# Kernel optimization log

Measured on AMD Instinct MI355X. Metric: run time of the kernel, lower is better.

The kernel has to match this reference:

```python
import jax, jax.numpy as jnp
import numpy as np

L = 30  # SSA window size (module default)


def _ssa_groups1(xm):
    """pyts-style SSA with groups=1: full-SVD reconstruction of the
    trajectory (Hankel) matrix followed by anti-diagonal averaging.
    xm: [B, N] -> [B, N]
    """
    B, N = xm.shape
    K = N - L + 1
    # Hankel trajectory matrix: X[b, i, j] = xm[b, i + j], shape [B, L, K]
    idx = jnp.arange(L)[:, None] + jnp.arange(K)[None, :]
    X = xm[:, idx]
    # SVD and rank-L reconstruction (groups=1 sums ALL elementary matrices)
    U, s, Vt = jnp.linalg.svd(X, full_matrices=False)  # U:[B,L,L] s:[B,L] Vt:[B,L,K]
    Xr = jnp.einsum('blr,br,brk->blk', U, s, Vt)       # [B, L, K]
    # Anti-diagonal (Hankel) averaging: average Xr[i, j] over i + j = t
    seg = idx.reshape(-1)                               # [L*K] values in [0, N)
    sums = jax.vmap(lambda m: jax.ops.segment_sum(m.reshape(-1), seg, num_segments=N))(Xr)
    counts = jax.ops.segment_sum(jnp.ones(L * K, dtype=xm.dtype), seg, num_segments=N)
    return sums / counts                                # [B, N]


def setup_inputs() -> dict:
    key = jax.random.key(0)
    x = jax.random.normal(key, (256, 64, 2048), dtype=jnp.float32)
    return {"x": x}


def reference(x):
    # x: [B, C, N]
    xm = jnp.max(x, axis=1)                 # channel-max, [B, N]
    x_ss = _ssa_groups1(xm)                 # SSA round-trip, [B, N]
    # Original code detaches the SSA branch (CPU/numpy round trip)
    x_ss = jax.lax.stop_gradient(x_ss)
    gate = jax.nn.softmax(x_ss, axis=-1)[:, None, :]  # [B, 1, N]
    return gate * x                         # [B, C, N]
```

## Files before the change

kernel.cpp:

```cpp
#include <hip/hip_runtime.h>
#include <math.h>


#define B_DIM 256
#define C_DIM 64
#define N_DIM 2048
#define COLS4 (N_DIM / 4)
#define ROW4  (C_DIM * COLS4)

__global__ __launch_bounds__(1024)
void gate_kernel(const float* __restrict__ x, float* __restrict__ out) {
    const int b    = blockIdx.x;
    const int t    = threadIdx.x;
    const int col  = t & (COLS4 - 1);
    const int grp  = t >> 9;
    const int lane = t & 63;
    const int wid  = t >> 6;

    const float4* __restrict__ xb = (const float4*)x + (size_t)b * ROW4;
    float4* ob = (float4*)out + (size_t)b * ROW4;

    __shared__ float4 pm[2][COLS4];
    __shared__ float  sred[16];

    const int c0 = grp * 32;
    float4 m = make_float4(-INFINITY, -INFINITY, -INFINITY, -INFINITY);
    #pragma unroll 8
    for (int c = 0; c < 32; ++c) {
        float4 v = xb[(size_t)(c0 + c) * COLS4 + col];
        m.x = fmaxf(m.x, v.x); m.y = fmaxf(m.y, v.y);
        m.z = fmaxf(m.z, v.z); m.w = fmaxf(m.w, v.w);
    }
    pm[grp][col] = m;
    __syncthreads();

    float4 e;
    if (t < COLS4) {
        float4 a  = pm[0][t];
        float4 c2 = pm[1][t];
        e.x = fmaxf(a.x, c2.x); e.y = fmaxf(a.y, c2.y);
        e.z = fmaxf(a.z, c2.z); e.w = fmaxf(a.w, c2.w);
        float tm = fmaxf(fmaxf(e.x, e.y), fmaxf(e.z, e.w));
        #pragma unroll
        for (int off = 32; off > 0; off >>= 1)
            tm = fmaxf(tm, __shfl_down(tm, off, 64));
        if (lane == 0) sred[wid] = tm;
    }
    __syncthreads();
    float M = sred[0];
    #pragma unroll
    for (int i = 1; i < 8; ++i) M = fmaxf(M, sred[i]);

    if (t < COLS4) {
        e.x = __expf(e.x - M); e.y = __expf(e.y - M);
        e.z = __expf(e.z - M); e.w = __expf(e.w - M);
        float ts = (e.x + e.y) + (e.z + e.w);
        #pragma unroll
        for (int off = 32; off > 0; off >>= 1)
            ts += __shfl_down(ts, off, 64);
        if (lane == 0) sred[8 + wid] = ts;
    }
    __syncthreads();

    if (t < COLS4) {
        float S = 0.0f;
        #pragma unroll
        for (int i = 8; i < 16; ++i) S += sred[i];
        const float inv = 1.0f / S;
        float4 gg;
        gg.x = e.x * inv; gg.y = e.y * inv; gg.z = e.z * inv; gg.w = e.w * inv;
        ob[(size_t)( 0) * COLS4 + t] = gg;
        ob[(size_t)(16) * COLS4 + t] = gg;
        ob[(size_t)(32) * COLS4 + t] = gg;
        ob[(size_t)(48) * COLS4 + t] = gg;
    }
}

__global__ __launch_bounds__(512)
void mul_kernel(const float* __restrict__ x, float* __restrict__ out) {
    const int bid = blockIdx.x;
    const int b   = bid >> 2;
    const int g   = bid & 3;
    const int col = threadIdx.x;

    const size_t rbase = (size_t)b * ROW4;
    const float4* __restrict__ x4 = (const float4*)x + rbase;
    float4* o4 = (float4*)out + rbase;

    const int cbase = g * 16;
    const float4 gv = o4[(size_t)cbase * COLS4 + col];
    __syncthreads();

    #pragma unroll 4
    for (int c = 0; c < 16; ++c) {
        const size_t idx = (size_t)(cbase + c) * COLS4 + col;
        float4 v = x4[idx];
        float4 o;
        o.x = v.x * gv.x; o.y = v.y * gv.y;
        o.z = v.z * gv.z; o.w = v.w * gv.w;
        o4[idx] = o;
    }
}

extern "C" void kernel_launch(void* const* d_in, const int* in_sizes, int n_in,
                              void* d_out, int out_size, void* d_ws, size_t ws_size,
                              hipStream_t stream) {
    const float* x = (const float*)d_in[0];
    float* out = (float*)d_out;
    gate_kernel<<<B_DIM, 1024, 0, stream>>>(x, out);
    mul_kernel<<<B_DIM * 4, 512, 0, stream>>>(x, out);
}
```

Measured before the change: 250.2 us.

## Fuse gate and multiply kernels, caching x in registers and LDS

```diff
diff --git a/kernel.cpp b/kernel.cpp
--- a/kernel.cpp
+++ b/kernel.cpp
@@ -8,97 +8,116 @@
 #define COLS4 (N_DIM / 4)
 #define ROW4  (C_DIM * COLS4)
 
-__global__ __launch_bounds__(1024)
-void gate_kernel(const float* __restrict__ x, float* __restrict__ out) {
+#define REGS_CH 16
+#define LDS_CH  3
+#define RR_CH   13
+
+__global__ __launch_bounds__(1024, 4)
+void ssa_gate_fused(const float* __restrict__ x, float* __restrict__ out) {
     const int b    = blockIdx.x;
     const int t    = threadIdx.x;
     const int col  = t & (COLS4 - 1);
     const int grp  = t >> 9;
     const int lane = t & 63;
     const int wid  = t >> 6;
+    const int c0   = grp * 32;
 
     const float4* __restrict__ xb = (const float4*)x + (size_t)b * ROW4;
-    float4* ob = (float4*)out + (size_t)b * ROW4;
+    float4* __restrict__ ob = (float4*)out + (size_t)b * ROW4;
 
-    __shared__ float4 pm[2][COLS4];
-    __shared__ float  sred[16];
+    __shared__ float4 ldsx[2][LDS_CH][COLS4];
+    __shared__ float4 xmbuf[COLS4];
+    __shared__ float  sredM[16];
+    __shared__ float  sredS[16];
 
-    const int c0 = grp * 32;
+    float4 r[REGS_CH];
     float4 m = make_float4(-INFINITY, -INFINITY, -INFINITY, -INFINITY);
-    #pragma unroll 8
-    for (int c = 0; c < 32; ++c) {
-        float4 v = xb[(size_t)(c0 + c) * COLS4 + col];
+    #pragma unroll
+    for (int c = 0; c < REGS_CH; ++c) {
+        r[c] = xb[(size_t)(c0 + c) * COLS4 + col];
+        m.x = fmaxf(m.x, r[c].x); m.y = fmaxf(m.y, r[c].y);
+        m.z = fmaxf(m.z, r[c].z); m.w = fmaxf(m.w, r[c].w);
+    }
+    #pragma unroll
+    for (int k = 0; k < LDS_CH; ++k) {
+        float4 v = xb[(size_t)(c0 + REGS_CH + k) * COLS4 + col];
+        ldsx[grp][k][col] = v;
         m.x = fmaxf(m.x, v.x); m.y = fmaxf(m.y, v.y);
         m.z = fmaxf(m.z, v.z); m.w = fmaxf(m.w, v.w);
     }
-    pm[grp][col] = m;
+    #pragma unroll
+    for (int k = 0; k < RR_CH; ++k) {
+        float4 v = xb[(size_t)(c0 + REGS_CH + LDS_CH + k) * COLS4 + col];
+        m.x = fmaxf(m.x, v.x); m.y = fmaxf(m.y, v.y);
+        m.z = fmaxf(m.z, v.z); m.w = fmaxf(m.w, v.w);
+    }
+
+    if (grp == 1) xmbuf[col] = m;
     __syncthreads();
 
     float4 e;
-    if (t < COLS4) {
-        float4 a  = pm[0][t];
-        float4 c2 = pm[1][t];
-        e.x = fmaxf(a.x, c2.x); e.y = fmaxf(a.y, c2.y);
-        e.z = fmaxf(a.z, c2.z); e.w = fmaxf(a.w, c2.w);
-        float tm = fmaxf(fmaxf(e.x, e.y), fmaxf(e.z, e.w));
-        #pragma unroll
-        for (int off = 32; off > 0; off >>= 1)
-            tm = fmaxf(tm, __shfl_down(tm, off, 64));
-        if (lane == 0) sred[wid] = tm;
+    float tm = -INFINITY;
+    if (grp == 0) {
+        float4 o = xmbuf[col];
+        e.x = fmaxf(m.x, o.x); e.y = fmaxf(m.y, o.y);
+        e.z = fmaxf(m.z, o.z); e.w = fmaxf(m.w, o.w);
+        tm = fmaxf(fmaxf(e.x, e.y), fmaxf(e.z, e.w));
+    }
+    #pragma unroll
+    for (int off = 32; off > 0; off >>= 1)
+        tm = fmaxf(tm, __shfl_down(tm, off, 64));
+    if (lane == 0) sredM[wid] = tm;
+    __syncthreads();
+    float M = sredM[0];
+    #pragma unroll
+    for (int i = 1; i < 16; ++i) M = fmaxf(M, sredM[i]);
+
+    float ts = 0.0f;
+    if (grp == 0) {
+        e.x = __expf(e.x - M); e.y = __expf(e.y - M);
+        e.z = __expf(e.z - M); e.w = __expf(e.w - M);
+        ts = (e.x + e.y) + (e.z + e.w);
+    }
+    #pragma unroll
+    for (int off = 32; off > 0; off >>= 1)
+        ts += __shfl_down(ts, off, 64);
+    if (lane == 0) sredS[wid] = ts;
+    __syncthreads();
+    float S = 0.0f;
+    #pragma unroll
+    for (int i = 0; i < 16; ++i) S += sredS[i];
+
+    if (grp == 0) {
+        const float inv = 1.0f / S;
+        float4 g;
+        g.x = e.x * inv; g.y = e.y * inv; g.z = e.z * inv; g.w = e.w * inv;
+        xmbuf[col] = g;
     }
     __syncthreads();
-    float M = sred[0];
+    const float4 g = xmbuf[col];
+
     #pragma unroll
-    for (int i = 1; i < 8; ++i) M = fmaxf(M, sred[i]);
-
-    if (t < COLS4) {
-        e.x = __expf(e.x - M); e.y = __expf(e.y - M);
-        e.z = __expf(e.z - M); e.w = __expf(e.w - M);
-        float ts = (e.x + e.y) + (e.z + e.w);
-        #pragma unroll
-        for (int off = 32; off > 0; off >>= 1)
-            ts += __shfl_down(ts, off, 64);
-        if (lane == 0) sred[8 + wid] = ts;
+    for (int c = 0; c < REGS_CH; ++c) {
+        float4 w;
+        w.x = r[c].x * g.x; w.y = r[c].y * g.y;
+        w.z = r[c].z * g.z; w.w = r[c].w * g.w;
+        ob[(size_t)(c0 + c) * COLS4 + col] = w;
     }
-    __syncthreads();
-
-    if (t < COLS4) {
-        float S = 0.0f;
-        #pragma unroll
-        for (int i = 8; i < 16; ++i) S += sred[i];
-        const float inv = 1.0f / S;
-        float4 gg;
-        gg.x = e.x * inv; gg.y = e.y * inv; gg.z = e.z * inv; gg.w = e.w * inv;
-        ob[(size_t)( 0) * COLS4 + t] = gg;
-        ob[(size_t)(16) * COLS4 + t] = gg;
-        ob[(size_t)(32) * COLS4 + t] = gg;
-        ob[(size_t)(48) * COLS4 + t] = gg;
+    #pragma unroll
+    for (int k = 0; k < LDS_CH; ++k) {
+        float4 v = ldsx[grp][k][col];
+        float4 w;
+        w.x = v.x * g.x; w.y = v.y * g.y;
+        w.z = v.z * g.z; w.w = v.w * g.w;
+        ob[(size_t)(c0 + REGS_CH + k) * COLS4 + col] = w;
     }
-}
-
-__global__ __launch_bounds__(512)
-void mul_kernel(const float* __restrict__ x, float* __restrict__ out) {
-    const int bid = blockIdx.x;
-    const int b   = bid >> 2;
-    const int g   = bid & 3;
-    const int col = threadIdx.x;
-
-    const size_t rbase = (size_t)b * ROW4;
-    const float4* __restrict__ x4 = (const float4*)x + rbase;
-    float4* o4 = (float4*)out + rbase;
-
-    const int cbase = g * 16;
-    const float4 gv = o4[(size_t)cbase * COLS4 + col];
-    __syncthreads();
-
-    #pragma unroll 4
-    for (int c = 0; c < 16; ++c) {
-        const size_t idx = (size_t)(cbase + c) * COLS4 + col;
-        float4 v = x4[idx];
-        float4 o;
-        o.x = v.x * gv.x; o.y = v.y * gv.y;
-        o.z = v.z * gv.z; o.w = v.w * gv.w;
-        o4[idx] = o;
+    #pragma unroll
+    for (int k = 0; k < RR_CH; ++k) {
+        float4 v = xb[(size_t)(c0 + REGS_CH + LDS_CH + k) * COLS4 + col];
+        float4 w;
+        w.x = v.x * g.x; w.y = v.y * g.y;
+        w.z = v.z * g.z; w.w = v.w * g.w;
+        ob[(size_t)(c0 + REGS_CH + LDS_CH + k) * COLS4 + col] = w;
     }
 }
 
@@ -107,6 +126,5 @@
                               hipStream_t stream) {
     const float* x = (const float*)d_in[0];
     float* out = (float*)d_out;
-    gate_kernel<<<B_DIM, 1024, 0, stream>>>(x, out);
-    mul_kernel<<<B_DIM * 4, 512, 0, stream>>>(x, out);
+    ssa_gate_fused<<<B_DIM, 1024, 0, stream>>>(x, out);
 }
```

Result: slower. 260.0 us (+3.9%).
